# Performance work log

Measured on AMD Instinct MI355X. Metric: run time of the kernel, lower is better.

## Reference

```python
import jax, jax.numpy as jnp
import numpy as np

N, E, C_IN, HID, CLASSES, K, G = 100000, 3200000, 3, 1024, 40, 5, 64
EPS = 1e-5


def setup_inputs() -> dict:
    key = jax.random.key(0)
    ks = jax.random.split(key, 8)
    pos = jax.random.normal(ks[0], (N, C_IN), jnp.float32)
    edge_index = jax.random.randint(ks[1], (2, E), 0, N, dtype=jnp.int64)
    batch = jnp.sort(jax.random.randint(ks[2], (N,), 0, G, dtype=jnp.int64))
    s = lambda k, sh: jax.random.normal(k, sh, jnp.float32) * 0.02
    return {
        "pos": pos, "edge_index": edge_index, "batch": batch,
        "lin_w": s(ks[3], (C_IN, HID)), "lin_b": jnp.zeros((HID,), jnp.float32),
        "bn0_g": jnp.ones((HID,), jnp.float32), "bn0_b": jnp.zeros((HID,), jnp.float32),
        "fc1_w": s(ks[4], (HID, 512)), "fc1_b": jnp.zeros((512,), jnp.float32),
        "bn1_g": jnp.ones((512,), jnp.float32), "bn1_b": jnp.zeros((512,), jnp.float32),
        "fc2_w": s(ks[5], (512, 256)), "fc2_b": jnp.zeros((256,), jnp.float32),
        "bn2_g": jnp.ones((256,), jnp.float32), "bn2_b": jnp.zeros((256,), jnp.float32),
        "fc3_w": s(ks[6], (256, CLASSES)), "fc3_b": jnp.zeros((CLASSES,), jnp.float32),
    }


def _bn(x, g, b):
    # BatchNorm1d in training mode: batch statistics over dim 0
    m = x.mean(0)
    v = x.var(0)
    return (x - m) * jax.lax.rsqrt(v + EPS) * g + b


def reference(pos, edge_index, batch, lin_w, lin_b, bn0_g, bn0_b,
              fc1_w, fc1_b, bn1_g, bn1_b, fc2_w, fc2_b, bn2_g, bn2_b,
              fc3_w, fc3_b):
    # --- SGConv: (D^-1/2 (A+I) D^-1/2)^K x, then Linear ---
    loops = jnp.arange(N, dtype=edge_index.dtype)
    row = jnp.concatenate([edge_index[0], loops])  # source nodes
    col = jnp.concatenate([edge_index[1], loops])  # target nodes
    deg = jax.ops.segment_sum(jnp.ones_like(row, jnp.float32), col, num_segments=N)
    dis = jax.lax.rsqrt(jnp.maximum(deg, 1.0))  # deg >= 1 due to self-loops
    norm = dis[row] * dis[col]                  # [E+N]
    x = pos
    for _ in range(K):
        x = jax.ops.segment_sum(norm[:, None] * x[row], col, num_segments=N)
    x = x @ lin_w + lin_b                        # [N, 1024]
    # --- BN + ReLU ---
    x = jax.nn.relu(_bn(x, bn0_g, bn0_b))
    # --- scatter_max pooling per graph ---
    pooled = jax.ops.segment_max(x, batch, num_segments=G)  # [G, 1024]
    # --- MLP head (dropout in eval = identity) ---
    h = jax.nn.relu(_bn(pooled @ fc1_w + fc1_b, bn1_g, bn1_b))
    h = jax.nn.relu(_bn(h @ fc2_w + fc2_b, bn2_g, bn2_b))
    return jax.nn.log_softmax(h @ fc3_w + fc3_b, axis=1)
```

## Files before the change

### kernel.cpp

```cpp
#include <hip/hip_runtime.h>
#include <math.h>

#define HID    1024
#define GG     64
#define KPROP  5
#define H1     512
#define H2     256
#define NCLS   40
#define BNEPS  1e-5f
#define TILE   2048
#define BPART  256
#define NBINS  1024
#define LDSCAP 8192

__host__ __device__ static inline int cdiv(int a, int b) { return (a + b - 1) / b; }

__global__ __launch_bounds__(1024) void k_hista(const int* __restrict__ col,
                                                int* __restrict__ blockHist, int e) {
    __shared__ int h[NBINS];
    for (int i = threadIdx.x; i < NBINS; i += 1024) h[i] = 0;
    __syncthreads();
    int chunk = cdiv(e, gridDim.x);
    int s = blockIdx.x * chunk, t = min(e, s + chunk);
    for (int i = s + threadIdx.x; i < t; i += 1024) atomicAdd(&h[col[i] >> 7], 1);
    __syncthreads();
    for (int i = threadIdx.x; i < NBINS; i += 1024)
        blockHist[blockIdx.x * NBINS + i] = h[i];
}

__global__ __launch_bounds__(1024) void k_scan(const int* __restrict__ blockHist,
                                               int* __restrict__ blockOff,
                                               int* __restrict__ bucketStart,
                                               int* __restrict__ rowptr, int e, int n) {
    __shared__ int tot[NBINS];
    int bin = threadIdx.x;
    int s = 0;
    for (int b = 0; b < BPART; b++) {
        int v = blockHist[b * NBINS + bin];
        blockOff[b * NBINS + bin] = s;
        s += v;
    }
    tot[bin] = s;
    __syncthreads();
    if (bin == 0) {
        int acc = 0;
        for (int i = 0; i < NBINS; i++) { int v = tot[i]; tot[i] = acc; acc += v; }
        rowptr[n] = e;
    }
    __syncthreads();
    bucketStart[bin] = tot[bin];
    if (bin == 0) bucketStart[NBINS] = e;
}

__global__ __launch_bounds__(1024) void k_scat(const int* __restrict__ row,
                                               const int* __restrict__ col,
                                               const int* __restrict__ blockOff,
                                               const int* __restrict__ bucketStart,
                                               int* __restrict__ ebuf, int e) {
    __shared__ int c2[NBINS];
    for (int i = threadIdx.x; i < NBINS; i += 1024) c2[i] = 0;
    __syncthreads();
    int chunk = cdiv(e, gridDim.x);
    int s = blockIdx.x * chunk, t = min(e, s + chunk);
    const int* boff = blockOff + blockIdx.x * NBINS;
    for (int i = s + threadIdx.x; i < t; i += 1024) {
        int c = col[i];
        int bin = c >> 7;
        int lr = atomicAdd(&c2[bin], 1);
        int pos = bucketStart[bin] + boff[bin] + lr;
        ebuf[pos] = row[i] | ((c & 127) << 17);
    }
}

__global__ __launch_bounds__(256) void k_csr(const int* __restrict__ bucketStart,
                                             int* __restrict__ ebuf,
                                             int* __restrict__ rowptr, int* __restrict__ deg,
                                             const float* __restrict__ pos,
                                             float4* __restrict__ z0, int n) {
    __shared__ int eb[LDSCAP];
    __shared__ int cnt[128];
    __shared__ int lptr[128];
    int g = blockIdx.x;
    int s0 = bucketStart[g], s1 = bucketStart[g + 1];
    int m = s1 - s0; if (m > LDSCAP) m = LDSCAP;
    for (int i = threadIdx.x; i < m; i += 256) eb[i] = ebuf[s0 + i];
    if (threadIdx.x < 128) cnt[threadIdx.x] = 0;
    __syncthreads();
    for (int i = threadIdx.x; i < m; i += 256) atomicAdd(&cnt[(eb[i] >> 17) & 127], 1);
    __syncthreads();
    if (threadIdx.x == 0) {
        int acc = 0;
        for (int i = 0; i < 128; i++) { lptr[i] = acc; acc += cnt[i]; }
    }
    __syncthreads();
    int node = g * 128 + threadIdx.x;
    if (threadIdx.x < 128 && node < n) {
        rowptr[node] = s0 + lptr[threadIdx.x];
        int d = cnt[threadIdx.x];
        deg[node] = d;
        float dis = rsqrtf((float)(d + 1));
        z0[node] = make_float4(dis * pos[3 * node], dis * pos[3 * node + 1],
                               dis * pos[3 * node + 2], 0.f);
    }
    if (threadIdx.x < 128) cnt[threadIdx.x] = 0;
    __syncthreads();
    for (int i = threadIdx.x; i < m; i += 256) {
        int v = eb[i];
        int t7 = (v >> 17) & 127;
        int slot = lptr[t7] + atomicAdd(&cnt[t7], 1);
        ebuf[s0 + slot] = v & 0x1FFFF;
    }
}

template <bool FINAL>
__global__ __launch_bounds__(256) void k_gather(
    const int* __restrict__ adj, const int* __restrict__ rowptr,
    const float4* __restrict__ zin, float4* __restrict__ zout,
    double* stats, int n) {
    int i = blockIdx.x * blockDim.x + threadIdx.x;
    float x0 = 0.f, x1 = 0.f, x2 = 0.f;
    if (i < n) {
        int s = rowptr[i], t = rowptr[i + 1];
        float4 zi = zin[i];
        float s0 = zi.x, s1 = zi.y, s2 = zi.z;
        float t0 = 0.f, t1 = 0.f, t2 = 0.f;
        int j = s;
        for (; j + 8 <= t; j += 8) {
            int4 qa = *(const int4*)(adj + j);
            int4 qb = *(const int4*)(adj + j + 4);
            float4 a = zin[qa.x], b = zin[qa.y], c = zin[qa.z], d = zin[qa.w];
            float4 p = zin[qb.x], q = zin[qb.y], r = zin[qb.z], u = zin[qb.w];
            s0 += a.x + b.x + c.x + d.x;
            s1 += a.y + b.y + c.y + d.y;
            s2 += a.z + b.z + c.z + d.z;
            t0 += p.x + q.x + r.x + u.x;
            t1 += p.y + q.y + r.y + u.y;
            t2 += p.z + q.z + r.z + u.z;
        }
        if (j + 4 <= t) {
            int4 qa = *(const int4*)(adj + j);
            float4 a = zin[qa.x], b = zin[qa.y], c = zin[qa.z], d = zin[qa.w];
            s0 += a.x + b.x + c.x + d.x;
            s1 += a.y + b.y + c.y + d.y;
            s2 += a.z + b.z + c.z + d.z;
            j += 4;
        }
        for (; j < t; j++) {
            float4 a = zin[adj[j]];
            s0 += a.x; s1 += a.y; s2 += a.z;
        }
        s0 += t0; s1 += t1; s2 += t2;
        float dg = (float)(t - s + 1);
        float sc = FINAL ? rsqrtf(dg) : (1.0f / dg);
        x0 = sc * s0; x1 = sc * s1; x2 = sc * s2;
        zout[i] = make_float4(x0, x1, x2, 0.f);
    }
    if (FINAL) {
        double v[9];
        v[0] = x0; v[1] = x1; v[2] = x2;
        v[3] = (double)x0 * x0; v[4] = (double)x0 * x1; v[5] = (double)x0 * x2;
        v[6] = (double)x1 * x1; v[7] = (double)x1 * x2; v[8] = (double)x2 * x2;
#pragma unroll
        for (int jj = 0; jj < 9; jj++) {
            double t = v[jj];
            for (int m = 1; m < 64; m <<= 1) t += __shfl_xor(t, m, 64);
            if ((threadIdx.x & 63) == 0) atomicAdd(&stats[jj], t);
        }
    }
}

__global__ void k_bounds(const int* __restrict__ batch, int* starts, int n) {
    int g = threadIdx.x;
    if (g <= GG) {
        int lo = 0, hi = n;
        while (lo < hi) {
            int mid = (lo + hi) >> 1;
            if (batch[mid] < g) lo = mid + 1; else hi = mid;
        }
        starts[g] = lo;
    }
}

__global__ __launch_bounds__(256) void k_pool(
    const float4* __restrict__ z, const int* __restrict__ starts,
    const float* __restrict__ lin_w,
    const float* __restrict__ bn0_g, const float* __restrict__ bn0_b,
    const double* __restrict__ stats, float* pooled, int n) {
    __shared__ float4 sh[TILE];
    int g = blockIdx.x;
    int c = blockIdx.y * 256 + threadIdx.x;

    float w0 = lin_w[c], w1 = lin_w[HID + c], w2 = lin_w[2 * HID + c];

    double invN = 1.0 / (double)n;
    double mu0 = stats[0] * invN, mu1 = stats[1] * invN, mu2 = stats[2] * invN;
    float c00 = (float)(stats[3] * invN - mu0 * mu0);
    float c01 = (float)(stats[4] * invN - mu0 * mu1);
    float c02 = (float)(stats[5] * invN - mu0 * mu2);
    float c11 = (float)(stats[6] * invN - mu1 * mu1);
    float c12 = (float)(stats[7] * invN - mu1 * mu2);
    float c22 = (float)(stats[8] * invN - mu2 * mu2);
    float meanc = (float)mu0 * w0 + (float)mu1 * w1 + (float)mu2 * w2;
    float var = c00 * w0 * w0 + c11 * w1 * w1 + c22 * w2 * w2
              + 2.f * (c01 * w0 * w1 + c02 * w0 * w2 + c12 * w1 * w2);
    var = fmaxf(var, 0.f);

    int s0 = starts[g], s1 = starts[g + 1];
    float mx = -INFINITY, mn = INFINITY;
    for (int base = s0; base < s1; base += TILE) {
        int cnt = min(TILE, s1 - base);
        __syncthreads();
        for (int j = threadIdx.x; j < cnt; j += 256) sh[j] = z[base + j];
        __syncthreads();
        for (int j = 0; j < cnt; j++) {
            float4 p = sh[j];
            float d = fmaf(p.x, w0, fmaf(p.y, w1, p.z * w2));
            mx = fmaxf(mx, d);
            mn = fminf(mn, d);
        }
    }
    float inv = rsqrtf(var + BNEPS);
    float s = bn0_g[c] * inv;
    float raw = (s >= 0.f) ? mx : mn;
    float y = (raw - meanc) * s + bn0_b[c];
    pooled[g * HID + c] = fmaxf(y, 0.f);
}

template <int KIN>
__global__ __launch_bounds__(64) void k_fcbn(
    const float* __restrict__ in, const float* __restrict__ W,
    const float* __restrict__ bias, const float* __restrict__ gamma,
    const float* __restrict__ beta, float* out, int Cout) {
    int c = blockIdx.x;
    int r = threadIdx.x;
    const float* rowp = in + r * KIN;
    float acc = 0.f;
#pragma unroll 8
    for (int k = 0; k < KIN; k++) acc = fmaf(rowp[k], W[k * Cout + c], acc);
    float y = acc + bias[c];
    float sum = y, sq = y * y;
    for (int m = 1; m < 64; m <<= 1) {
        sum += __shfl_xor(sum, m, 64);
        sq  += __shfl_xor(sq, m, 64);
    }
    float mean = sum * (1.f / 64.f);
    float var  = fmaxf(sq * (1.f / 64.f) - mean * mean, 0.f);
    float o = (y - mean) * rsqrtf(var + BNEPS) * gamma[c] + beta[c];
    out[r * Cout + c] = fmaxf(o, 0.f);
}

__global__ __launch_bounds__(64) void k_out(
    const float* __restrict__ in, const float* __restrict__ W,
    const float* __restrict__ bias, float* out) {
    int r = blockIdx.x;
    int c = threadIdx.x;
    bool act = c < NCLS;
    float z = -INFINITY;
    if (act) {
        const float* rowp = in + r * H2;
        float acc = 0.f;
#pragma unroll 8
        for (int k = 0; k < H2; k++) acc = fmaf(rowp[k], W[k * NCLS + c], acc);
        z = acc + bias[c];
    }
    float mx = z;
    for (int m = 1; m < 64; m <<= 1) mx = fmaxf(mx, __shfl_xor(mx, m, 64));
    float ex = act ? expf(z - mx) : 0.f;
    float se = ex;
    for (int m = 1; m < 64; m <<= 1) se += __shfl_xor(se, m, 64);
    if (act) out[r * NCLS + c] = z - mx - logf(se);
}

extern "C" void kernel_launch(void* const* d_in, const int* in_sizes, int n_in,
                              void* d_out, int out_size, void* d_ws, size_t ws_size,
                              hipStream_t stream) {
    const float* pos   = (const float*)d_in[0];
    const int*   ei    = (const int*)d_in[1];
    const int*   batch = (const int*)d_in[2];
    const float* lin_w = (const float*)d_in[3];
    const float* bn0_g = (const float*)d_in[5];
    const float* bn0_b = (const float*)d_in[6];
    const float* fc1_w = (const float*)d_in[7];
    const float* fc1_b = (const float*)d_in[8];
    const float* bn1_g = (const float*)d_in[9];
    const float* bn1_b = (const float*)d_in[10];
    const float* fc2_w = (const float*)d_in[11];
    const float* fc2_b = (const float*)d_in[12];
    const float* bn2_g = (const float*)d_in[13];
    const float* bn2_b = (const float*)d_in[14];
    const float* fc3_w = (const float*)d_in[15];
    const float* fc3_b = (const float*)d_in[16];

    int n = in_sizes[0] / 3;
    int e = in_sizes[1] / 2;
    int nbuck = cdiv(n, 128);

    auto align256 = [](size_t x) { return (x + 255) & ~(size_t)255; };
    char* w = (char*)d_ws;
    int*    blockHist = (int*)w;    w += align256((size_t)BPART * NBINS * 4);
    int*    blockOff  = (int*)w;    w += align256((size_t)BPART * NBINS * 4);
    int*    bucketSt  = (int*)w;    w += align256((NBINS + 1) * 4);
    int*    rowptr    = (int*)w;    w += align256((size_t)(n + 1) * 4);
    int*    deg       = (int*)w;    w += align256((size_t)n * 4);
    int*    ebuf      = (int*)w;    w += align256((size_t)e * 4);
    float4* za        = (float4*)w; w += align256((size_t)n * 16);
    float4* zb        = (float4*)w; w += align256((size_t)n * 16);
    double* stats     = (double*)w; w += align256(9 * sizeof(double));
    int*    starts    = (int*)w;    w += align256((GG + 1) * 4);
    float*  pooled    = (float*)w;  w += align256((size_t)GG * HID * 4);
    float*  h1        = (float*)w;  w += align256((size_t)GG * H1 * 4);
    float*  h2        = (float*)w;  w += align256((size_t)GG * H2 * 4);

    (void)hipMemsetAsync(stats, 0, 9 * sizeof(double), stream);

    const int* erow = ei;
    const int* ecol = ei + e;

    k_hista<<<BPART, 1024, 0, stream>>>(ecol, blockHist, e);
    k_scan <<<1, NBINS, 0, stream>>>(blockHist, blockOff, bucketSt, rowptr, e, n);
    k_scat <<<BPART, 1024, 0, stream>>>(erow, ecol, blockOff, bucketSt, ebuf, e);
    k_csr  <<<nbuck, 256, 0, stream>>>(bucketSt, ebuf, rowptr, deg, pos, za, n);

    int gn = cdiv(n, 256);
    k_gather<false><<<gn, 256, 0, stream>>>(ebuf, rowptr, za, zb, stats, n);
    k_gather<false><<<gn, 256, 0, stream>>>(ebuf, rowptr, zb, za, stats, n);
    k_gather<false><<<gn, 256, 0, stream>>>(ebuf, rowptr, za, zb, stats, n);
    k_gather<false><<<gn, 256, 0, stream>>>(ebuf, rowptr, zb, za, stats, n);
    k_gather<true ><<<gn, 256, 0, stream>>>(ebuf, rowptr, za, zb, stats, n);

    k_bounds<<<1, 128, 0, stream>>>(batch, starts, n);
    k_pool<<<dim3(GG, HID / 256), 256, 0, stream>>>(zb, starts, lin_w, bn0_g, bn0_b, stats, pooled, n);
    k_fcbn<HID><<<H1, 64, 0, stream>>>(pooled, fc1_w, fc1_b, bn1_g, bn1_b, h1, H1);
    k_fcbn<H1><<<H2, 64, 0, stream>>>(h1, fc2_w, fc2_b, bn2_g, bn2_b, h2, H2);
    k_out<<<GG, 64, 0, stream>>>(h2, fc3_w, fc3_b, (float*)d_out);
}
```

Baseline: 563.5 us.

## Replace per-node CSR gather with source-tiled LDS propagation and LDS atomic accumulation

The per-node CSR gather, which does random global float4 loads of neighbour features, is replaced by a tiled scheme. Edges inside each 128-node target bucket are sorted by source tile of 8192 nodes. Each block streams every source tile into LDS and accumulates into per-target LDS buffers with atomics. This aims to turn scattered global reads into LDS reads. In exchange, every block must load all source tiles (about 13 tiles, 128KB of LDS), grid size is capped at 256 blocks, and the LDS float atomics may contend on hot targets.

```diff
diff --git a/kernel.cpp b/kernel.cpp
--- a/kernel.cpp
+++ b/kernel.cpp
@@ -12,6 +12,10 @@
 #define BPART  256
 #define NBINS  1024
 #define LDSCAP 8192
+#define TS     8192
+#define TSH    13
+#define MAXB   4
+#define TPS    20
 
 __host__ __device__ static inline int cdiv(int a, int b) { return (a + b - 1) / b; }
 
@@ -30,8 +34,7 @@
 
 __global__ __launch_bounds__(1024) void k_scan(const int* __restrict__ blockHist,
                                                int* __restrict__ blockOff,
-                                               int* __restrict__ bucketStart,
-                                               int* __restrict__ rowptr, int e, int n) {
+                                               int* __restrict__ bucketStart, int e) {
     __shared__ int tot[NBINS];
     int bin = threadIdx.x;
     int s = 0;
@@ -45,7 +48,6 @@
     if (bin == 0) {
         int acc = 0;
         for (int i = 0; i < NBINS; i++) { int v = tot[i]; tot[i] = acc; acc += v; }
-        rowptr[n] = e;
     }
     __syncthreads();
     bucketStart[bin] = tot[bin];
@@ -74,97 +76,116 @@
 
 __global__ __launch_bounds__(256) void k_csr(const int* __restrict__ bucketStart,
                                              int* __restrict__ ebuf,
-                                             int* __restrict__ rowptr, int* __restrict__ deg,
+                                             int* __restrict__ tptr, int* __restrict__ deg,
                                              const float* __restrict__ pos,
-                                             float4* __restrict__ z0, int n) {
+                                             float4* __restrict__ z0, int n, int ntiles) {
     __shared__ int eb[LDSCAP];
     __shared__ int cnt[128];
-    __shared__ int lptr[128];
+    __shared__ int tc[17];
+    __shared__ int tp[17];
     int g = blockIdx.x;
     int s0 = bucketStart[g], s1 = bucketStart[g + 1];
     int m = s1 - s0; if (m > LDSCAP) m = LDSCAP;
     for (int i = threadIdx.x; i < m; i += 256) eb[i] = ebuf[s0 + i];
     if (threadIdx.x < 128) cnt[threadIdx.x] = 0;
-    __syncthreads();
-    for (int i = threadIdx.x; i < m; i += 256) atomicAdd(&cnt[(eb[i] >> 17) & 127], 1);
+    if (threadIdx.x < 17) tc[threadIdx.x] = 0;
+    __syncthreads();
+    for (int i = threadIdx.x; i < m; i += 256) {
+        int v = eb[i];
+        atomicAdd(&cnt[(v >> 17) & 127], 1);
+        atomicAdd(&tc[(v & 0x1FFFF) >> TSH], 1);
+    }
     __syncthreads();
     if (threadIdx.x == 0) {
         int acc = 0;
-        for (int i = 0; i < 128; i++) { lptr[i] = acc; acc += cnt[i]; }
-    }
-    __syncthreads();
+        for (int i = 0; i < ntiles; i++) { tp[i] = acc; acc += tc[i]; }
+        tp[ntiles] = acc;
+    }
+    __syncthreads();
+    if (threadIdx.x <= ntiles) tptr[g * TPS + threadIdx.x] = s0 + tp[threadIdx.x];
     int node = g * 128 + threadIdx.x;
     if (threadIdx.x < 128 && node < n) {
-        rowptr[node] = s0 + lptr[threadIdx.x];
         int d = cnt[threadIdx.x];
         deg[node] = d;
         float dis = rsqrtf((float)(d + 1));
         z0[node] = make_float4(dis * pos[3 * node], dis * pos[3 * node + 1],
                                dis * pos[3 * node + 2], 0.f);
     }
-    if (threadIdx.x < 128) cnt[threadIdx.x] = 0;
+    if (threadIdx.x < 17) tc[threadIdx.x] = 0;
     __syncthreads();
     for (int i = threadIdx.x; i < m; i += 256) {
         int v = eb[i];
-        int t7 = (v >> 17) & 127;
-        int slot = lptr[t7] + atomicAdd(&cnt[t7], 1);
-        ebuf[s0 + slot] = v & 0x1FFFF;
+        int t = (v & 0x1FFFF) >> TSH;
+        int slot = tp[t] + atomicAdd(&tc[t], 1);
+        ebuf[s0 + slot] = v;
     }
 }
 
 template <bool FINAL>
-__global__ __launch_bounds__(256) void k_gather(
-    const int* __restrict__ adj, const int* __restrict__ rowptr,
-    const float4* __restrict__ zin, float4* __restrict__ zout,
-    double* stats, int n) {
-    int i = blockIdx.x * blockDim.x + threadIdx.x;
-    float x0 = 0.f, x1 = 0.f, x2 = 0.f;
-    if (i < n) {
-        int s = rowptr[i], t = rowptr[i + 1];
-        float4 zi = zin[i];
-        float s0 = zi.x, s1 = zi.y, s2 = zi.z;
-        float t0 = 0.f, t1 = 0.f, t2 = 0.f;
-        int j = s;
-        for (; j + 8 <= t; j += 8) {
-            int4 qa = *(const int4*)(adj + j);
-            int4 qb = *(const int4*)(adj + j + 4);
-            float4 a = zin[qa.x], b = zin[qa.y], c = zin[qa.z], d = zin[qa.w];
-            float4 p = zin[qb.x], q = zin[qb.y], r = zin[qb.z], u = zin[qb.w];
-            s0 += a.x + b.x + c.x + d.x;
-            s1 += a.y + b.y + c.y + d.y;
-            s2 += a.z + b.z + c.z + d.z;
-            t0 += p.x + q.x + r.x + u.x;
-            t1 += p.y + q.y + r.y + u.y;
-            t2 += p.z + q.z + r.z + u.z;
-        }
-        if (j + 4 <= t) {
-            int4 qa = *(const int4*)(adj + j);
-            float4 a = zin[qa.x], b = zin[qa.y], c = zin[qa.z], d = zin[qa.w];
-            s0 += a.x + b.x + c.x + d.x;
-            s1 += a.y + b.y + c.y + d.y;
-            s2 += a.z + b.z + c.z + d.z;
-            j += 4;
-        }
-        for (; j < t; j++) {
-            float4 a = zin[adj[j]];
-            s0 += a.x; s1 += a.y; s2 += a.z;
-        }
-        s0 += t0; s1 += t1; s2 += t2;
-        float dg = (float)(t - s + 1);
-        float sc = FINAL ? rsqrtf(dg) : (1.0f / dg);
-        x0 = sc * s0; x1 = sc * s1; x2 = sc * s2;
-        zout[i] = make_float4(x0, x1, x2, 0.f);
+__global__ __launch_bounds__(256) void k_gt(
+    const int* __restrict__ ebuf, const int* __restrict__ tptr,
+    const int* __restrict__ deg, const float4* __restrict__ zin,
+    float4* __restrict__ zout, double* __restrict__ stats,
+    int n, int nbuck, int nblk, int ntiles) {
+    __shared__ float4 zt[TS];
+    __shared__ float acc[MAXB * 384];
+    long long bx = blockIdx.x;
+    int b0 = (int)(bx * nbuck / nblk);
+    int b1 = (int)((bx + 1) * nbuck / nblk);
+    int nb = b1 - b0;
+    for (int i = threadIdx.x; i < nb * 384; i += 256) acc[i] = 0.f;
+    for (int t = 0; t < ntiles; t++) {
+        int base = t << TSH;
+        int cnt = min(TS, n - base);
+        for (int i = threadIdx.x; i < cnt; i += 256) zt[i] = zin[base + i];
+        __syncthreads();
+        for (int bi = 0; bi < nb; bi++) {
+            int g = b0 + bi;
+            int es = tptr[g * TPS + t];
+            int ee = tptr[g * TPS + t + 1];
+            float* ab = acc + bi * 384;
+            for (int idx = es + threadIdx.x; idx < ee; idx += 256) {
+                int v = ebuf[idx];
+                int tgt = (v >> 17) & 127;
+                float4 z = zt[(v & 0x1FFFF) - base];
+                atomicAdd(&ab[tgt], z.x);
+                atomicAdd(&ab[128 + tgt], z.y);
+                atomicAdd(&ab[256 + tgt], z.z);
+            }
+        }
+        __syncthreads();
+    }
+    double v[9];
+#pragma unroll
+    for (int jj = 0; jj < 9; jj++) v[jj] = 0.0;
+    if (threadIdx.x < 128) {
+        for (int bi = 0; bi < nb; bi++) {
+            int node = (b0 + bi) * 128 + threadIdx.x;
+            if (node < n) {
+                float4 zi = zin[node];
+                float* ab = acc + bi * 384;
+                float s0 = ab[threadIdx.x] + zi.x;
+                float s1 = ab[128 + threadIdx.x] + zi.y;
+                float s2 = ab[256 + threadIdx.x] + zi.z;
+                float dg = (float)(deg[node] + 1);
+                float sc = FINAL ? rsqrtf(dg) : (1.f / dg);
+                float x0 = sc * s0, x1 = sc * s1, x2 = sc * s2;
+                zout[node] = make_float4(x0, x1, x2, 0.f);
+                if (FINAL) {
+                    v[0] += x0; v[1] += x1; v[2] += x2;
+                    v[3] += (double)x0 * x0; v[4] += (double)x0 * x1;
+                    v[5] += (double)x0 * x2; v[6] += (double)x1 * x1;
+                    v[7] += (double)x1 * x2; v[8] += (double)x2 * x2;
+                }
+            }
+        }
     }
     if (FINAL) {
-        double v[9];
-        v[0] = x0; v[1] = x1; v[2] = x2;
-        v[3] = (double)x0 * x0; v[4] = (double)x0 * x1; v[5] = (double)x0 * x2;
-        v[6] = (double)x1 * x1; v[7] = (double)x1 * x2; v[8] = (double)x2 * x2;
 #pragma unroll
         for (int jj = 0; jj < 9; jj++) {
-            double t = v[jj];
-            for (int m = 1; m < 64; m <<= 1) t += __shfl_xor(t, m, 64);
-            if ((threadIdx.x & 63) == 0) atomicAdd(&stats[jj], t);
+            double tt = v[jj];
+            for (int m = 1; m < 64; m <<= 1) tt += __shfl_xor(tt, m, 64);
+            if ((threadIdx.x & 63) == 0) atomicAdd(&stats[jj], tt);
         }
     }
 }
@@ -294,13 +315,15 @@
     int n = in_sizes[0] / 3;
     int e = in_sizes[1] / 2;
     int nbuck = cdiv(n, 128);
+    int ntiles = cdiv(n, TS);
+    int nblk = min(256, nbuck);
 
     auto align256 = [](size_t x) { return (x + 255) & ~(size_t)255; };
     char* w = (char*)d_ws;
     int*    blockHist = (int*)w;    w += align256((size_t)BPART * NBINS * 4);
     int*    blockOff  = (int*)w;    w += align256((size_t)BPART * NBINS * 4);
     int*    bucketSt  = (int*)w;    w += align256((NBINS + 1) * 4);
-    int*    rowptr    = (int*)w;    w += align256((size_t)(n + 1) * 4);
+    int*    tptr      = (int*)w;    w += align256((size_t)nbuck * TPS * 4);
     int*    deg       = (int*)w;    w += align256((size_t)n * 4);
     int*    ebuf      = (int*)w;    w += align256((size_t)e * 4);
     float4* za        = (float4*)w; w += align256((size_t)n * 16);
@@ -317,16 +340,15 @@
     const int* ecol = ei + e;
 
     k_hista<<<BPART, 1024, 0, stream>>>(ecol, blockHist, e);
-    k_scan <<<1, NBINS, 0, stream>>>(blockHist, blockOff, bucketSt, rowptr, e, n);
+    k_scan <<<1, NBINS, 0, stream>>>(blockHist, blockOff, bucketSt, e);
     k_scat <<<BPART, 1024, 0, stream>>>(erow, ecol, blockOff, bucketSt, ebuf, e);
-    k_csr  <<<nbuck, 256, 0, stream>>>(bucketSt, ebuf, rowptr, deg, pos, za, n);
-
-    int gn = cdiv(n, 256);
-    k_gather<false><<<gn, 256, 0, stream>>>(ebuf, rowptr, za, zb, stats, n);
-    k_gather<false><<<gn, 256, 0, stream>>>(ebuf, rowptr, zb, za, stats, n);
-    k_gather<false><<<gn, 256, 0, stream>>>(ebuf, rowptr, za, zb, stats, n);
-    k_gather<false><<<gn, 256, 0, stream>>>(ebuf, rowptr, zb, za, stats, n);
-    k_gather<true ><<<gn, 256, 0, stream>>>(ebuf, rowptr, za, zb, stats, n);
+    k_csr  <<<nbuck, 256, 0, stream>>>(bucketSt, ebuf, tptr, deg, pos, za, n, ntiles);
+
+    k_gt<false><<<nblk, 256, 0, stream>>>(ebuf, tptr, deg, za, zb, stats, n, nbuck, nblk, ntiles);
+    k_gt<false><<<nblk, 256, 0, stream>>>(ebuf, tptr, deg, zb, za, stats, n, nbuck, nblk, ntiles);
+    k_gt<false><<<nblk, 256, 0, stream>>>(ebuf, tptr, deg, za, zb, stats, n, nbuck, nblk, ntiles);
+    k_gt<false><<<nblk, 256, 0, stream>>>(ebuf, tptr, deg, zb, za, stats, n, nbuck, nblk, ntiles);
+    k_gt<true ><<<nblk, 256, 0, stream>>>(ebuf, tptr, deg, za, zb, stats, n, nbuck, nblk, ntiles);
 
     k_bounds<<<1, 128, 0, stream>>>(batch, starts, n);
     k_pool<<<dim3(GG, HID / 256), 256, 0, stream>>>(zb, starts, lin_w, bn0_g, bn0_b, stats, pooled, n);
```

Result: slower. 1.211 ms (+114.9%).

## Replace pull-gather SpMV with source-sorted expand plus contiguous CSR reduce

Applied to the files above, without the earlier changes.

Propagation changes from a per-node random gather of neighbour features into two phases. An expand kernel reads source features in source-sorted order and scatters them to their final CSR slot in a 16-byte-per-edge value buffer. A reduce kernel then sums each node's contiguous values. This needs a second counting sort by source and a slot map from the CSR build, and it writes and reads 16 bytes per edge per iteration instead of 4-byte indices plus random 16-byte reads. The partition count also drops from 256 to 64 blocks.

```diff
diff --git a/kernel.cpp b/kernel.cpp
--- a/kernel.cpp
+++ b/kernel.cpp
@@ -9,20 +9,22 @@
 #define NCLS   40
 #define BNEPS  1e-5f
 #define TILE   2048
-#define BPART  256
+#define BPART  64
 #define NBINS  1024
 #define LDSCAP 8192
 
+typedef float v4f __attribute__((ext_vector_type(4)));
+
 __host__ __device__ static inline int cdiv(int a, int b) { return (a + b - 1) / b; }
 
-__global__ __launch_bounds__(1024) void k_hista(const int* __restrict__ col,
+__global__ __launch_bounds__(1024) void k_hista(const int* __restrict__ key,
                                                 int* __restrict__ blockHist, int e) {
     __shared__ int h[NBINS];
     for (int i = threadIdx.x; i < NBINS; i += 1024) h[i] = 0;
     __syncthreads();
     int chunk = cdiv(e, gridDim.x);
     int s = blockIdx.x * chunk, t = min(e, s + chunk);
-    for (int i = s + threadIdx.x; i < t; i += 1024) atomicAdd(&h[col[i] >> 7], 1);
+    for (int i = s + threadIdx.x; i < t; i += 1024) atomicAdd(&h[key[i] >> 7], 1);
     __syncthreads();
     for (int i = threadIdx.x; i < NBINS; i += 1024)
         blockHist[blockIdx.x * NBINS + i] = h[i];
@@ -56,7 +58,8 @@
                                                const int* __restrict__ col,
                                                const int* __restrict__ blockOff,
                                                const int* __restrict__ bucketStart,
-                                               int* __restrict__ ebuf, int e) {
+                                               int* __restrict__ ebuf,
+                                               int* __restrict__ eorig, int e) {
     __shared__ int c2[NBINS];
     for (int i = threadIdx.x; i < NBINS; i += 1024) c2[i] = 0;
     __syncthreads();
@@ -69,21 +72,25 @@
         int lr = atomicAdd(&c2[bin], 1);
         int pos = bucketStart[bin] + boff[bin] + lr;
         ebuf[pos] = row[i] | ((c & 127) << 17);
+        eorig[pos] = i;
     }
 }
 
 __global__ __launch_bounds__(256) void k_csr(const int* __restrict__ bucketStart,
-                                             int* __restrict__ ebuf,
-                                             int* __restrict__ rowptr, int* __restrict__ deg,
+                                             const int* __restrict__ ebuf,
+                                             const int* __restrict__ eorig,
+                                             int* __restrict__ rowptr,
+                                             int* __restrict__ finalslot,
                                              const float* __restrict__ pos,
                                              float4* __restrict__ z0, int n) {
     __shared__ int eb[LDSCAP];
+    __shared__ int eo[LDSCAP];
     __shared__ int cnt[128];
     __shared__ int lptr[128];
     int g = blockIdx.x;
     int s0 = bucketStart[g], s1 = bucketStart[g + 1];
     int m = s1 - s0; if (m > LDSCAP) m = LDSCAP;
-    for (int i = threadIdx.x; i < m; i += 256) eb[i] = ebuf[s0 + i];
+    for (int i = threadIdx.x; i < m; i += 256) { eb[i] = ebuf[s0 + i]; eo[i] = eorig[s0 + i]; }
     if (threadIdx.x < 128) cnt[threadIdx.x] = 0;
     __syncthreads();
     for (int i = threadIdx.x; i < m; i += 256) atomicAdd(&cnt[(eb[i] >> 17) & 127], 1);
@@ -96,27 +103,58 @@
     int node = g * 128 + threadIdx.x;
     if (threadIdx.x < 128 && node < n) {
         rowptr[node] = s0 + lptr[threadIdx.x];
-        int d = cnt[threadIdx.x];
-        deg[node] = d;
-        float dis = rsqrtf((float)(d + 1));
+        float dis = rsqrtf((float)(cnt[threadIdx.x] + 1));
         z0[node] = make_float4(dis * pos[3 * node], dis * pos[3 * node + 1],
                                dis * pos[3 * node + 2], 0.f);
     }
     if (threadIdx.x < 128) cnt[threadIdx.x] = 0;
     __syncthreads();
     for (int i = threadIdx.x; i < m; i += 256) {
-        int v = eb[i];
-        int t7 = (v >> 17) & 127;
+        int t7 = (eb[i] >> 17) & 127;
         int slot = lptr[t7] + atomicAdd(&cnt[t7], 1);
-        ebuf[s0 + slot] = v & 0x1FFFF;
+        finalslot[eo[i]] = s0 + slot;
+    }
+}
+
+__global__ __launch_bounds__(1024) void k_scatb(const int* __restrict__ row,
+                                                const int* __restrict__ finalslot,
+                                                const int* __restrict__ blockOffB,
+                                                const int* __restrict__ bucketStB,
+                                                int* __restrict__ osrc,
+                                                int* __restrict__ oslot, int e) {
+    __shared__ int c2[NBINS];
+    for (int i = threadIdx.x; i < NBINS; i += 1024) c2[i] = 0;
+    __syncthreads();
+    int chunk = cdiv(e, gridDim.x);
+    int s = blockIdx.x * chunk, t = min(e, s + chunk);
+    const int* boff = blockOffB + blockIdx.x * NBINS;
+    for (int i = s + threadIdx.x; i < t; i += 1024) {
+        int r = row[i];
+        int bin = r >> 7;
+        int lr = atomicAdd(&c2[bin], 1);
+        int pos = bucketStB[bin] + boff[bin] + lr;
+        osrc[pos] = r;
+        oslot[pos] = finalslot[i];
+    }
+}
+
+__global__ __launch_bounds__(256) void k_expand(const int* __restrict__ osrc,
+                                                const int* __restrict__ oslot,
+                                                const v4f* __restrict__ zin,
+                                                v4f* __restrict__ val, int e) {
+    int i = blockIdx.x * blockDim.x + threadIdx.x;
+    if (i < e) {
+        v4f z = zin[osrc[i]];
+        __builtin_nontemporal_store(z, val + oslot[i]);
     }
 }
 
 template <bool FINAL>
-__global__ __launch_bounds__(256) void k_gather(
-    const int* __restrict__ adj, const int* __restrict__ rowptr,
-    const float4* __restrict__ zin, float4* __restrict__ zout,
-    double* stats, int n) {
+__global__ __launch_bounds__(256) void k_reduce(const int* __restrict__ rowptr,
+                                                const v4f* __restrict__ val,
+                                                const float4* __restrict__ zin,
+                                                float4* __restrict__ zout,
+                                                double* __restrict__ stats, int n) {
     int i = blockIdx.x * blockDim.x + threadIdx.x;
     float x0 = 0.f, x1 = 0.f, x2 = 0.f;
     if (i < n) {
@@ -126,10 +164,8 @@
         float t0 = 0.f, t1 = 0.f, t2 = 0.f;
         int j = s;
         for (; j + 8 <= t; j += 8) {
-            int4 qa = *(const int4*)(adj + j);
-            int4 qb = *(const int4*)(adj + j + 4);
-            float4 a = zin[qa.x], b = zin[qa.y], c = zin[qa.z], d = zin[qa.w];
-            float4 p = zin[qb.x], q = zin[qb.y], r = zin[qb.z], u = zin[qb.w];
+            v4f a = val[j],     b = val[j + 1], c = val[j + 2], d = val[j + 3];
+            v4f p = val[j + 4], q = val[j + 5], r = val[j + 6], u = val[j + 7];
             s0 += a.x + b.x + c.x + d.x;
             s1 += a.y + b.y + c.y + d.y;
             s2 += a.z + b.z + c.z + d.z;
@@ -138,15 +174,14 @@
             t2 += p.z + q.z + r.z + u.z;
         }
         if (j + 4 <= t) {
-            int4 qa = *(const int4*)(adj + j);
-            float4 a = zin[qa.x], b = zin[qa.y], c = zin[qa.z], d = zin[qa.w];
+            v4f a = val[j], b = val[j + 1], c = val[j + 2], d = val[j + 3];
             s0 += a.x + b.x + c.x + d.x;
             s1 += a.y + b.y + c.y + d.y;
             s2 += a.z + b.z + c.z + d.z;
             j += 4;
         }
         for (; j < t; j++) {
-            float4 a = zin[adj[j]];
+            v4f a = val[j];
             s0 += a.x; s1 += a.y; s2 += a.z;
         }
         s0 += t0; s1 += t1; s2 += t2;
@@ -299,10 +334,17 @@
     char* w = (char*)d_ws;
     int*    blockHist = (int*)w;    w += align256((size_t)BPART * NBINS * 4);
     int*    blockOff  = (int*)w;    w += align256((size_t)BPART * NBINS * 4);
+    int*    blockOffB = (int*)w;    w += align256((size_t)BPART * NBINS * 4);
     int*    bucketSt  = (int*)w;    w += align256((NBINS + 1) * 4);
+    int*    bucketStB = (int*)w;    w += align256((NBINS + 1) * 4);
     int*    rowptr    = (int*)w;    w += align256((size_t)(n + 1) * 4);
-    int*    deg       = (int*)w;    w += align256((size_t)n * 4);
-    int*    ebuf      = (int*)w;    w += align256((size_t)e * 4);
+    char*   valbase   = w;          w += align256((size_t)e * 16);
+    int*    ebuf      = (int*)valbase;
+    int*    eorig     = (int*)(valbase + (size_t)e * 4);
+    int*    finalslot = (int*)(valbase + (size_t)e * 8);
+    v4f*    val       = (v4f*)valbase;
+    int*    osrc      = (int*)w;    w += align256((size_t)e * 4);
+    int*    oslot     = (int*)w;    w += align256((size_t)e * 4);
     float4* za        = (float4*)w; w += align256((size_t)n * 16);
     float4* zb        = (float4*)w; w += align256((size_t)n * 16);
     double* stats     = (double*)w; w += align256(9 * sizeof(double));
@@ -318,17 +360,28 @@
 
     k_hista<<<BPART, 1024, 0, stream>>>(ecol, blockHist, e);
     k_scan <<<1, NBINS, 0, stream>>>(blockHist, blockOff, bucketSt, rowptr, e, n);
-    k_scat <<<BPART, 1024, 0, stream>>>(erow, ecol, blockOff, bucketSt, ebuf, e);
-    k_csr  <<<nbuck, 256, 0, stream>>>(bucketSt, ebuf, rowptr, deg, pos, za, n);
-
+    k_scat <<<BPART, 1024, 0, stream>>>(erow, ecol, blockOff, bucketSt, ebuf, eorig, e);
+    k_csr  <<<nbuck, 256, 0, stream>>>(bucketSt, ebuf, eorig, rowptr, finalslot, pos, za, n);
+
+    k_hista<<<BPART, 1024, 0, stream>>>(erow, blockHist, e);
+    k_scan <<<1, NBINS, 0, stream>>>(blockHist, blockOffB, bucketStB, rowptr, e, n);
+    k_scatb<<<BPART, 1024, 0, stream>>>(erow, finalslot, blockOffB, bucketStB, osrc, oslot, e);
+
+    k_bounds<<<1, 128, 0, stream>>>(batch, starts, n);
+
+    int ge = cdiv(e, 256);
     int gn = cdiv(n, 256);
-    k_gather<false><<<gn, 256, 0, stream>>>(ebuf, rowptr, za, zb, stats, n);
-    k_gather<false><<<gn, 256, 0, stream>>>(ebuf, rowptr, zb, za, stats, n);
-    k_gather<false><<<gn, 256, 0, stream>>>(ebuf, rowptr, za, zb, stats, n);
-    k_gather<false><<<gn, 256, 0, stream>>>(ebuf, rowptr, zb, za, stats, n);
-    k_gather<true ><<<gn, 256, 0, stream>>>(ebuf, rowptr, za, zb, stats, n);
-
-    k_bounds<<<1, 128, 0, stream>>>(batch, starts, n);
+    k_expand<<<ge, 256, 0, stream>>>(osrc, oslot, (const v4f*)za, val, e);
+    k_reduce<false><<<gn, 256, 0, stream>>>(rowptr, val, za, zb, stats, n);
+    k_expand<<<ge, 256, 0, stream>>>(osrc, oslot, (const v4f*)zb, val, e);
+    k_reduce<false><<<gn, 256, 0, stream>>>(rowptr, val, zb, za, stats, n);
+    k_expand<<<ge, 256, 0, stream>>>(osrc, oslot, (const v4f*)za, val, e);
+    k_reduce<false><<<gn, 256, 0, stream>>>(rowptr, val, za, zb, stats, n);
+    k_expand<<<ge, 256, 0, stream>>>(osrc, oslot, (const v4f*)zb, val, e);
+    k_reduce<false><<<gn, 256, 0, stream>>>(rowptr, val, zb, za, stats, n);
+    k_expand<<<ge, 256, 0, stream>>>(osrc, oslot, (const v4f*)za, val, e);
+    k_reduce<true ><<<gn, 256, 0, stream>>>(rowptr, val, za, zb, stats, n);
+
     k_pool<<<dim3(GG, HID / 256), 256, 0, stream>>>(zb, starts, lin_w, bn0_g, bn0_b, stats, pooled, n);
     k_fcbn<HID><<<H1, 64, 0, stream>>>(pooled, fc1_w, fc1_b, bn1_g, bn1_b, h1, H1);
     k_fcbn<H1><<<H2, 64, 0, stream>>>(h1, fc2_w, fc2_b, bn2_g, bn2_b, h2, H2);
```

Result: slower. 1.366 ms (+142.5%).
